# Performance work log

Hardware: AMD Instinct MI355X
Metric: run time of the kernel (lower is better)

The kernel has to match this reference:

```python
import jax, jax.numpy as jnp
import numpy as np

B, S, D, HD = 4, 4096, 1024, 64

def setup_inputs() -> dict:
    key = jax.random.key(0)
    ks = jax.random.split(key, 4)
    scale = 1.0 / np.sqrt(D)
    return {
        "x": jax.random.normal(ks[0], (B, S, D), dtype=jnp.float32),
        "wq": jax.random.normal(ks[1], (HD, D), dtype=jnp.float32) * scale,
        "bq": jnp.zeros((HD,), dtype=jnp.float32),
        "wk": jax.random.normal(ks[2], (HD, D), dtype=jnp.float32) * scale,
        "bk": jnp.zeros((HD,), dtype=jnp.float32),
        "wv": jax.random.normal(ks[3], (HD, D), dtype=jnp.float32) * scale,
        "bv": jnp.zeros((HD,), dtype=jnp.float32),
    }

def reference(x, wq, bq, wk, bk, wv, bv):
    seq_len = x.shape[1]
    head_dim = wq.shape[0]
    # projections: nn.Linear stores weight as [out, in]
    q = jnp.einsum('bsd,hd->bsh', x, wq) + bq  # [B,S,HD]
    k = jnp.einsum('bsd,hd->bsh', x, wk) + bk
    v = jnp.einsum('bsd,hd->bsh', x, wv) + bv
    score = jnp.einsum('bqh,bkh->bqk', q, k) / jnp.sqrt(jnp.float32(head_dim))  # [B,S,S]
    causal = jnp.tril(jnp.ones((seq_len, seq_len), dtype=bool))
    score = jnp.where(causal, score, -jnp.inf)
    attn = jax.nn.softmax(score, axis=-1)
    # dropout p=0.0 -> identity
    out = jnp.einsum('bqk,bkh->bqh', attn, v)  # [B,S,HD]
    return out
```

## Files before the change

### kernel.cpp

```cpp
#include <hip/hip_runtime.h>
#include <math.h>

#define B_   4
#define S_   4096
#define D_   1024
#define HD_  64

#define CK            8
#define CHUNKS_PER_B  288
#define FULL_CHUNKS   224
#define PSTRIDE_SH    72
#define SLOT_SH       (64 * PSTRIDE_SH)

#define QSCALE   (0.125f * 1.44269504089f)

typedef float  f32x4  __attribute__((ext_vector_type(4)));
typedef __bf16 bf16x8 __attribute__((ext_vector_type(8)));
typedef __bf16 bf16x4 __attribute__((ext_vector_type(4)));

static __device__ __forceinline__ unsigned short bfbits(float f) {
    __bf16 h = (__bf16)f;
    return __builtin_bit_cast(unsigned short, h);
}

static __device__ __forceinline__ float exp2_hw(float x) {
    return __builtin_exp2f(x);
}

static __device__ __forceinline__ int chunk_slot(int qi, int c) {
    const int a = qi >> 3, r = qi & 7;
    return qi + 4 * a * (a - 1) + a * r + c;
}

__global__ __launch_bounds__(256) void convert_w(
    const float* __restrict__ wq, const float* __restrict__ wk,
    const float* __restrict__ wv, unsigned short* __restrict__ wbf)
{
    const int col = blockIdx.x;
    const int p = col >> 6, h = col & 63;
    const float* src = (p == 0 ? wq : (p == 1 ? wk : wv)) + (size_t)h * D_;
    const int t = threadIdx.x;
    const float4 v = ((const float4*)src)[t];
    bf16x4 o;
    o[0] = (__bf16)v.x; o[1] = (__bf16)v.y; o[2] = (__bf16)v.z; o[3] = (__bf16)v.w;
    *(bf16x4*)&wbf[(size_t)col * D_ + 4 * t] = o;
}

__global__ __launch_bounds__(256) void proj_mfma(
    const float* __restrict__ x, const unsigned short* __restrict__ wbf,
    const float* __restrict__ bq, const float* __restrict__ bk,
    const float* __restrict__ bv,
    unsigned short* __restrict__ qbf, unsigned short* __restrict__ kbf,
    unsigned short* __restrict__ vtb)
{
    __shared__ unsigned short xs[32][136];
    __shared__ unsigned short wsh[96][136];

    const int t = threadIdx.x;
    const int w = t >> 6, lane = t & 63;
    const int n = lane & 15, g = lane >> 4;
    const int koff = 8 * g;
    const int rt = w & 1, cg = w >> 1;
    const size_t row0 = (size_t)blockIdx.x * 32;
    const int colbase = 96 * blockIdx.y;

    f32x4 acc[3];
#pragma unroll
    for (int i = 0; i < 3; ++i) acc[i] = (f32x4)0.f;

    for (int chunk = 0; chunk < 8; ++chunk) {
        const int d0 = chunk * 128;
        __syncthreads();
#pragma unroll
        for (int i = 0; i < 4; ++i) {
            int e = t + i * 256;
            int r = e >> 5, c4 = (e & 31) * 4;
            float4 v = *(const float4*)&x[(row0 + r) * D_ + d0 + c4];
            bf16x4 o;
            o[0] = (__bf16)v.x; o[1] = (__bf16)v.y;
            o[2] = (__bf16)v.z; o[3] = (__bf16)v.w;
            *(bf16x4*)&xs[r][c4] = o;
        }
#pragma unroll
        for (int i = 0; i < 6; ++i) {
            int e = t + i * 256;
            int col = e >> 4, g8 = (e & 15) * 8;
            uint4 v = *(const uint4*)&wbf[(size_t)(colbase + col) * D_ + d0 + g8];
            *(uint4*)&wsh[col][g8] = v;
        }
        __syncthreads();

#pragma unroll
        for (int ks = 0; ks < 4; ++ks) {
            const int k0 = 32 * ks;
            const bf16x8 a = *(const bf16x8*)&xs[16 * rt + n][k0 + koff];
#pragma unroll
            for (int ci = 0; ci < 3; ++ci) {
                const bf16x8 b = *(const bf16x8*)&wsh[48 * cg + 16 * ci + n][k0 + koff];
                acc[ci] = __builtin_amdgcn_mfma_f32_16x16x32_bf16(a, b, acc[ci], 0, 0, 0);
            }
        }
    }

#pragma unroll
    for (int ci = 0; ci < 3; ++ci) {
        const int gct = 6 * blockIdx.y + 3 * cg + ci;
        const int p = gct >> 2, h0 = (gct & 3) * 16;
        const int h = h0 + n;
        const float bb = (p == 0 ? bq : (p == 1 ? bk : bv))[h];
        if (p == 2) {
            const size_t grow0 = row0 + 16 * rt + 4 * g;
            const int bidx = (int)(grow0 >> 12);
            const int s0 = (int)(grow0 & 4095);
            bf16x4 u;
            u[0] = (__bf16)(acc[ci][0] + bb); u[1] = (__bf16)(acc[ci][1] + bb);
            u[2] = (__bf16)(acc[ci][2] + bb); u[3] = (__bf16)(acc[ci][3] + bb);
            *(bf16x4*)&vtb[((size_t)bidx * HD_ + h) * S_ + s0] = u;
        } else {
            unsigned short* outp = (p == 0 ? qbf : kbf);
            const float scale = (p == 0) ? QSCALE : 1.0f;
#pragma unroll
            for (int r = 0; r < 4; ++r) {
                const size_t grow = row0 + 16 * rt + 4 * g + r;
                outp[grow * HD_ + h] = bfbits((acc[ci][r] + bb) * scale);
            }
        }
    }
}

__global__ __launch_bounds__(256) void flash_splitk(
    const unsigned short* __restrict__ qg, const unsigned short* __restrict__ kg,
    const unsigned short* __restrict__ vt, float* __restrict__ out,
    unsigned short* __restrict__ part)
{
    __shared__ unsigned short qsh[64][72];
    __shared__ unsigned short ksh[64][72];
    __shared__ unsigned short vsh[64][72];
    __shared__ unsigned short psh[4][16][72];

    const int t    = threadIdx.x;
    const int w    = t >> 6;
    const int lane = t & 63;
    const int n    = lane & 15;
    const int g    = lane >> 4;
    const int koff = 8 * g;

    int b, qi, c;
    {
        const int idx = blockIdx.x;
        if (idx < B_ * FULL_CHUNKS) {
            b = idx / FULL_CHUNKS;
            int rem = idx - b * FULL_CHUNKS;
            qi = 8;
            while (rem >= (qi >> 3)) { rem -= (qi >> 3); ++qi; }
            c = rem;
        } else {
            const int r2 = idx - B_ * FULL_CHUNKS;
            b = r2 >> 6;
            qi = r2 & 63;
            c = qi >> 3;
        }
    }
    const int kt0 = c * CK;
    const int kt1 = min(qi, kt0 + CK - 1);
    const int nc  = (qi >> 3) + 1;

    const size_t qtile = ((size_t)b * S_ + (size_t)qi * 64) * HD_;

    {
        const uint4* src = (const uint4*)(qg + qtile);
#pragma unroll
        for (int i = 0; i < 2; ++i) {
            int e = t + i * 256;
            int r = e >> 3, gg = e & 7;
            *(uint4*)&qsh[r][8 * gg] = src[e];
        }
    }

    const int r0s = t >> 3,        gg0 = t & 7;
    const int r1s = (t + 256) >> 3, gg1 = (t + 256) & 7;

    uint4 kr0, kr1, vr0, vr1;
    {
        const size_t kvb = ((size_t)b * S_ + (size_t)kt0 * 64) * HD_;
        const uint4* ksrc = (const uint4*)(kg + kvb);
        kr0 = ksrc[t];
        kr1 = ksrc[t + 256];
        vr0 = *(const uint4*)&vt[((size_t)b * HD_ + r0s) * S_ + kt0 * 64 + 8 * gg0];
        vr1 = *(const uint4*)&vt[((size_t)b * HD_ + r1s) * S_ + kt0 * 64 + 8 * gg1];
    }

    f32x4 o4[4];
#pragma unroll
    for (int i = 0; i < 4; ++i) o4[i] = (f32x4)0.f;
    float m_r = -INFINITY, l_r = 0.f;

    for (int kt = kt0; kt <= kt1; ++kt) {
        __syncthreads();
        *(uint4*)&ksh[r0s][8 * gg0] = kr0;
        *(uint4*)&ksh[r1s][8 * gg1] = kr1;
        *(uint4*)&vsh[r0s][8 * gg0] = vr0;
        *(uint4*)&vsh[r1s][8 * gg1] = vr1;
        __syncthreads();

        if (kt < kt1) {
            const size_t kvb = ((size_t)b * S_ + (size_t)(kt + 1) * 64) * HD_;
            const uint4* ksrc = (const uint4*)(kg + kvb);
            kr0 = ksrc[t];
            kr1 = ksrc[t + 256];
            vr0 = *(const uint4*)&vt[((size_t)b * HD_ + r0s) * S_ + (kt + 1) * 64 + 8 * gg0];
            vr1 = *(const uint4*)&vt[((size_t)b * HD_ + r1s) * S_ + (kt + 1) * 64 + 8 * gg1];
        }

        f32x4 sc[4];
#pragma unroll
        for (int mt = 0; mt < 4; ++mt) sc[mt] = (f32x4)0.f;
#pragma unroll
        for (int ks = 0; ks < 2; ++ks) {
            const bf16x8 bq8 = *(const bf16x8*)&qsh[16 * w + n][32 * ks + koff];
#pragma unroll
            for (int mt = 0; mt < 4; ++mt) {
                const bf16x8 ak = *(const bf16x8*)&ksh[16 * mt + n][32 * ks + koff];
                sc[mt] = __builtin_amdgcn_mfma_f32_16x16x32_bf16(ak, bq8, sc[mt], 0, 0, 0);
            }
        }

        if (kt == qi) {
            const int qloc = 16 * w + n;
#pragma unroll
            for (int mt = 0; mt < 4; ++mt)
#pragma unroll
                for (int r = 0; r < 4; ++r) {
                    const int kloc = 16 * mt + 4 * g + r;
                    if (kloc > qloc) sc[mt][r] = -INFINITY;
                }
        }

        float mx = -INFINITY;
#pragma unroll
        for (int mt = 0; mt < 4; ++mt)
#pragma unroll
            for (int r = 0; r < 4; ++r) mx = fmaxf(mx, sc[mt][r]);
        mx = fmaxf(mx, __shfl_xor(mx, 16));
        mx = fmaxf(mx, __shfl_xor(mx, 32));

        const float m_new = fmaxf(m_r, mx);
        const float alpha = exp2_hw(m_r - m_new);
        float psum = 0.f;
#pragma unroll
        for (int mt = 0; mt < 4; ++mt)
#pragma unroll
            for (int r = 0; r < 4; ++r) {
                const float pe = exp2_hw(sc[mt][r] - m_new);
                sc[mt][r] = pe;
                psum += pe;
            }
        psum += __shfl_xor(psum, 16);
        psum += __shfl_xor(psum, 32);
        l_r = l_r * alpha + psum;
        m_r = m_new;

#pragma unroll
        for (int ht = 0; ht < 4; ++ht)
#pragma unroll
            for (int r = 0; r < 4; ++r) o4[ht][r] *= alpha;

#pragma unroll
        for (int mt = 0; mt < 4; ++mt) {
            bf16x4 u;
            u[0] = (__bf16)sc[mt][0]; u[1] = (__bf16)sc[mt][1];
            u[2] = (__bf16)sc[mt][2]; u[3] = (__bf16)sc[mt][3];
            *(bf16x4*)&psh[w][n][16 * mt + 4 * g] = u;
        }

#pragma unroll
        for (int ks = 0; ks < 2; ++ks) {
            const bf16x8 ap = *(const bf16x8*)&psh[w][n][32 * ks + koff];
#pragma unroll
            for (int ht = 0; ht < 4; ++ht) {
                const bf16x8 av = *(const bf16x8*)&vsh[16 * ht + n][32 * ks + koff];
                o4[ht] = __builtin_amdgcn_mfma_f32_16x16x32_bf16(av, ap, o4[ht], 0, 0, 0);
            }
        }
    }

    const size_t qbase = ((size_t)b * S_ + (size_t)qi * 64) * HD_;
    if (nc == 1) {
        const float inv = 1.f / l_r;
        const size_t ob = qbase + (size_t)(16 * w + n) * HD_;
#pragma unroll
        for (int ht = 0; ht < 4; ++ht) {
            float4 rv;
            rv.x = o4[ht][0] * inv; rv.y = o4[ht][1] * inv;
            rv.z = o4[ht][2] * inv; rv.w = o4[ht][3] * inv;
            *(float4*)&out[ob + 16 * ht + 4 * g] = rv;
        }
    } else {
        const size_t sb = ((size_t)b * CHUNKS_PER_B + chunk_slot(qi, c)) * SLOT_SH;
        const size_t pb = sb + (size_t)(16 * w + n) * PSTRIDE_SH;
#pragma unroll
        for (int ht = 0; ht < 4; ++ht) {
            bf16x4 u;
            u[0] = (__bf16)o4[ht][0]; u[1] = (__bf16)o4[ht][1];
            u[2] = (__bf16)o4[ht][2]; u[3] = (__bf16)o4[ht][3];
            *(bf16x4*)&part[pb + 16 * ht + 4 * g] = u;
        }
        if (g == 0) {
            *(float*)&part[pb + 64] = m_r;
            *(float*)&part[pb + 66] = l_r;
        }
    }
}

__global__ __launch_bounds__(256) void combine(
    const unsigned short* __restrict__ part, float* __restrict__ out)
{
    const int t  = threadIdx.x;
    const int qr = t >> 2, tc = t & 3;
    const int qi = blockIdx.x + CK;
    const int b  = blockIdx.y;
    const int hq = blockIdx.z;
    const int nc = (qi >> 3) + 1;

    const size_t base0 = ((size_t)b * CHUNKS_PER_B + chunk_slot(qi, 0)) * SLOT_SH
                       + (size_t)qr * PSTRIDE_SH;

    float M = -INFINITY;
    for (int c0 = 0; c0 < nc; ++c0)
        M = fmaxf(M, *(const float*)&part[base0 + (size_t)c0 * SLOT_SH + 64]);

    float L = 0.f;
    float o[4];
#pragma unroll
    for (int j = 0; j < 4; ++j) o[j] = 0.f;

    const int ho = hq * 16 + tc * 4;

    for (int c0 = 0; c0 < nc; ++c0) {
        const size_t sb = base0 + (size_t)c0 * SLOT_SH;
        const float m_c = *(const float*)&part[sb + 64];
        const float l_c = *(const float*)&part[sb + 66];
        const float w = exp2_hw(m_c - M);
        L += w * l_c;
        const bf16x4 ov = *(const bf16x4*)&part[sb + ho];
#pragma unroll
        for (int j = 0; j < 4; ++j) o[j] += w * (float)ov[j];
    }

    const float inv = 1.f / L;
    const size_t ob = ((size_t)b * S_ + (size_t)qi * 64 + qr) * HD_ + ho;
    float4 r;
    r.x = o[0] * inv; r.y = o[1] * inv; r.z = o[2] * inv; r.w = o[3] * inv;
    *(float4*)&out[ob] = r;
}

extern "C" void kernel_launch(void* const* d_in, const int* in_sizes, int n_in,
                              void* d_out, int out_size, void* d_ws, size_t ws_size,
                              hipStream_t stream)
{
    const float* x  = (const float*)d_in[0];
    const float* wq = (const float*)d_in[1];
    const float* bq = (const float*)d_in[2];
    const float* wk = (const float*)d_in[3];
    const float* bk = (const float*)d_in[4];
    const float* wv = (const float*)d_in[5];
    const float* bv = (const float*)d_in[6];
    float* outp = (float*)d_out;

    const size_t n = (size_t)B_ * S_ * HD_;
    unsigned short* qbf = (unsigned short*)d_ws;
    unsigned short* kbf = qbf + n;
    unsigned short* vtb = kbf + n;
    unsigned short* wbf = vtb + n;
    unsigned short* part = wbf + (size_t)192 * D_;

    convert_w<<<dim3(192), 256, 0, stream>>>(wq, wk, wv, wbf);
    proj_mfma<<<dim3(B_ * S_ / 32, 2), 256, 0, stream>>>(
        x, wbf, bq, bk, bv, qbf, kbf, vtb);
    flash_splitk<<<dim3(B_ * CHUNKS_PER_B), 256, 0, stream>>>(
        qbf, kbf, vtb, outp, part);
    combine<<<dim3(S_ / 64 - CK, B_, 4), 256, 0, stream>>>(part, outp);
}
```

Before: 153.4 us.

## Swizzle shared K/V/P tiles, keep Q in registers, raise occupancy bound

Replaces the padded shared-memory tiles with unpadded 64-wide rows using an XOR swizzle on 16-byte groups, which is meant to avoid LDS bank conflicts without padding. Q fragments are loaded straight from global memory into registers, so the Q shared tile and its per-iteration LDS reads go away. The launch bounds now request 6 blocks per SM; the smaller LDS footprint makes that more reachable, but the hint may force register spills.

```diff
diff --git a/kernel.cpp b/kernel.cpp
--- a/kernel.cpp
+++ b/kernel.cpp
@@ -128,22 +128,21 @@
     }
 }
 
-__global__ __launch_bounds__(256) void flash_splitk(
+__global__ __launch_bounds__(256, 6) void flash_splitk(
     const unsigned short* __restrict__ qg, const unsigned short* __restrict__ kg,
     const unsigned short* __restrict__ vt, float* __restrict__ out,
     unsigned short* __restrict__ part)
 {
-    __shared__ unsigned short qsh[64][72];
-    __shared__ unsigned short ksh[64][72];
-    __shared__ unsigned short vsh[64][72];
-    __shared__ unsigned short psh[4][16][72];
+    __shared__ unsigned short ksh[64 * 64];
+    __shared__ unsigned short vsh[64 * 64];
+    __shared__ unsigned short psh[4 * 16 * 64];
 
     const int t    = threadIdx.x;
     const int w    = t >> 6;
     const int lane = t & 63;
     const int n    = lane & 15;
     const int g    = lane >> 4;
-    const int koff = 8 * g;
+    const int nx   = n & 7;
 
     int b, qi, c;
     {
@@ -167,18 +166,17 @@
 
     const size_t qtile = ((size_t)b * S_ + (size_t)qi * 64) * HD_;
 
+    bf16x8 q8[2];
     {
-        const uint4* src = (const uint4*)(qg + qtile);
-#pragma unroll
-        for (int i = 0; i < 2; ++i) {
-            int e = t + i * 256;
-            int r = e >> 3, gg = e & 7;
-            *(uint4*)&qsh[r][8 * gg] = src[e];
-        }
-    }
-
-    const int r0s = t >> 3,        gg0 = t & 7;
-    const int r1s = (t + 256) >> 3, gg1 = (t + 256) & 7;
+        const unsigned short* qrow = qg + qtile + (size_t)(16 * w + n) * HD_ + 8 * g;
+        q8[0] = *(const bf16x8*)&qrow[0];
+        q8[1] = *(const bf16x8*)&qrow[32];
+    }
+
+    const int r0s = t >> 3,       gg0 = t & 7;
+    const int r1s = r0s + 32;
+    const int so0 = r0s * 64 + ((gg0 ^ (r0s & 7)) << 3);
+    const int so1 = r1s * 64 + ((gg0 ^ (r1s & 7)) << 3);
 
     uint4 kr0, kr1, vr0, vr1;
     {
@@ -187,7 +185,7 @@
         kr0 = ksrc[t];
         kr1 = ksrc[t + 256];
         vr0 = *(const uint4*)&vt[((size_t)b * HD_ + r0s) * S_ + kt0 * 64 + 8 * gg0];
-        vr1 = *(const uint4*)&vt[((size_t)b * HD_ + r1s) * S_ + kt0 * 64 + 8 * gg1];
+        vr1 = *(const uint4*)&vt[((size_t)b * HD_ + r1s) * S_ + kt0 * 64 + 8 * gg0];
     }
 
     f32x4 o4[4];
@@ -197,10 +195,10 @@
 
     for (int kt = kt0; kt <= kt1; ++kt) {
         __syncthreads();
-        *(uint4*)&ksh[r0s][8 * gg0] = kr0;
-        *(uint4*)&ksh[r1s][8 * gg1] = kr1;
-        *(uint4*)&vsh[r0s][8 * gg0] = vr0;
-        *(uint4*)&vsh[r1s][8 * gg1] = vr1;
+        *(uint4*)&ksh[so0] = kr0;
+        *(uint4*)&ksh[so1] = kr1;
+        *(uint4*)&vsh[so0] = vr0;
+        *(uint4*)&vsh[so1] = vr1;
         __syncthreads();
 
         if (kt < kt1) {
@@ -209,7 +207,7 @@
             kr0 = ksrc[t];
             kr1 = ksrc[t + 256];
             vr0 = *(const uint4*)&vt[((size_t)b * HD_ + r0s) * S_ + (kt + 1) * 64 + 8 * gg0];
-            vr1 = *(const uint4*)&vt[((size_t)b * HD_ + r1s) * S_ + (kt + 1) * 64 + 8 * gg1];
+            vr1 = *(const uint4*)&vt[((size_t)b * HD_ + r1s) * S_ + (kt + 1) * 64 + 8 * gg0];
         }
 
         f32x4 sc[4];
@@ -217,11 +215,11 @@
         for (int mt = 0; mt < 4; ++mt) sc[mt] = (f32x4)0.f;
 #pragma unroll
         for (int ks = 0; ks < 2; ++ks) {
-            const bf16x8 bq8 = *(const bf16x8*)&qsh[16 * w + n][32 * ks + koff];
 #pragma unroll
             for (int mt = 0; mt < 4; ++mt) {
-                const bf16x8 ak = *(const bf16x8*)&ksh[16 * mt + n][32 * ks + koff];
-                sc[mt] = __builtin_amdgcn_mfma_f32_16x16x32_bf16(ak, bq8, sc[mt], 0, 0, 0);
+                const bf16x8 ak = *(const bf16x8*)&ksh[1024 * mt + 64 * n
+                                                      + (((4 * ks + g) ^ nx) << 3)];
+                sc[mt] = __builtin_amdgcn_mfma_f32_16x16x32_bf16(ak, q8[ks], sc[mt], 0, 0, 0);
             }
         }
 
@@ -270,15 +268,18 @@
             bf16x4 u;
             u[0] = (__bf16)sc[mt][0]; u[1] = (__bf16)sc[mt][1];
             u[2] = (__bf16)sc[mt][2]; u[3] = (__bf16)sc[mt][3];
-            *(bf16x4*)&psh[w][n][16 * mt + 4 * g] = u;
+            *(bf16x4*)&psh[1024 * w + 64 * n + (((2 * mt + (g >> 1)) ^ nx) << 3)
+                           + ((g & 1) << 2)] = u;
         }
 
 #pragma unroll
         for (int ks = 0; ks < 2; ++ks) {
-            const bf16x8 ap = *(const bf16x8*)&psh[w][n][32 * ks + koff];
+            const bf16x8 ap = *(const bf16x8*)&psh[1024 * w + 64 * n
+                                                   + (((4 * ks + g) ^ nx) << 3)];
 #pragma unroll
             for (int ht = 0; ht < 4; ++ht) {
-                const bf16x8 av = *(const bf16x8*)&vsh[16 * ht + n][32 * ks + koff];
+                const bf16x8 av = *(const bf16x8*)&vsh[1024 * ht + 64 * n
+                                                       + (((4 * ks + g) ^ nx) << 3)];
                 o4[ht] = __builtin_amdgcn_mfma_f32_16x16x32_bf16(av, ap, o4[ht], 0, 0, 0);
             }
         }
```

After: 173.5 us. 13.1% more time.
